# Optimization experiments

Hardware: AMD Instinct MI355X
Metric: run time of the kernel (lower is better)

## Reference

```python
import jax, jax.numpy as jnp
import numpy as np
from jax import lax

B, H, W, CIN = 32, 64, 64, 128
F, KH, KW = 256, 3, 3
NCLS = 10


def setup_inputs() -> dict:
    key = jax.random.key(0)
    k1, k2, k3, k4 = jax.random.split(key, 4)
    x = jax.random.normal(k1, (B, H, W, CIN), dtype=jnp.float32)
    classes = jax.random.randint(k2, (B, 1), 0, NCLS, dtype=jnp.int32)
    kernel = jax.random.normal(k3, (NCLS, KH, KW, CIN, F), dtype=jnp.float32) * 0.05
    bias = jax.random.normal(k4, (NCLS, F), dtype=jnp.float32) * 0.05
    return {"x": x, "classes": classes, "kernel": kernel, "bias": bias}


def reference(x, classes, kernel, bias):
    # classes: [B,1] -> [B]
    cls = jnp.squeeze(classes, axis=1)
    k_per = kernel[cls]   # [B, KH, KW, CIN, F] per-sample gathered expert kernel
    b_per = bias[cls]     # [B, F]

    def conv_one(xi, ki):
        # xi: [H,W,CIN], ki: [KH,KW,CIN,F]
        y = lax.conv_general_dilated(
            xi[None], ki,
            window_strides=(1, 1),
            padding="SAME",
            rhs_dilation=(1, 1),
            dimension_numbers=("NHWC", "HWIO", "NHWC"),
        )
        return y[0]

    out = jax.vmap(conv_one)(x, k_per)          # [B,H,W,F]
    out = out + b_per[:, None, None, :]
    return out
```

## Files before the change

kernel.cpp:

```cpp
#include <hip/hip_runtime.h>
#include <stdint.h>

#define BATCH 32
#define CINX 128
#define FOUT 256
#define NCLS 10

typedef __bf16 bf16x8 __attribute__((ext_vector_type(8)));
typedef float f32x4 __attribute__((ext_vector_type(4)));

#define WT_SLAB 32768
#define WT_BYTES ((size_t)NCLS * 9 * WT_SLAB * 2)
#define Z_BYTES 4096
#define X16_BYTES ((size_t)BATCH * 4096 * CINX * 2)
#define WS_NEED (WT_BYTES + Z_BYTES + X16_BYTES)

#define BAR() __builtin_amdgcn_s_barrier()
#define SCHEDBAR() __builtin_amdgcn_sched_barrier(0)
#define VMW4() asm volatile("s_waitcnt vmcnt(4)" ::: "memory")
#define VMW0() asm volatile("s_waitcnt vmcnt(0)" ::: "memory")

__device__ __forceinline__ void gl16(const void* g, void* l) {
    __builtin_amdgcn_global_load_lds(
        (const __attribute__((address_space(1))) void*)g,
        (__attribute__((address_space(3))) void*)l, 16, 0, 0);
}

__global__ __launch_bounds__(256) void prep_all(const float* __restrict__ kin,
                                                __bf16* __restrict__ wt,
                                                const float* __restrict__ x,
                                                __bf16* __restrict__ x16,
                                                __bf16* __restrict__ zbuf) {
    if (blockIdx.x < NCLS * 9) {
        __shared__ __bf16 tile[128 * 260];
        const int slab = blockIdx.x;
        const float* src = kin + (size_t)slab * (CINX * FOUT);
        __bf16* dst = wt + (size_t)slab * WT_SLAB;
        const int t = threadIdx.x;
#pragma unroll
        for (int i = 0; i < 32; ++i) {
            int e4 = t + i * 256;
            int c = e4 >> 6, f4 = e4 & 63;
            f32x4 v = *(const f32x4*)(src + (size_t)e4 * 4);
            __bf16* p = &tile[c * 260 + f4 * 4];
            p[0] = (__bf16)v[0]; p[1] = (__bf16)v[1];
            p[2] = (__bf16)v[2]; p[3] = (__bf16)v[3];
        }
        __syncthreads();
#pragma unroll
        for (int i = 0; i < 16; ++i) {
            int g = t + i * 256;
            int c32 = g >> 10;
            int u = g & 1023;
            int f = u >> 2, slot = u & 3;
            int cu = slot ^ ((f >> 1) & 3);
            int c0 = c32 * 32 + cu * 8;
            bf16x8 o;
#pragma unroll
            for (int j = 0; j < 8; ++j) o[j] = tile[(c0 + j) * 260 + f];
            *(bf16x8*)(dst + (size_t)g * 8) = o;
        }
    } else {
        const int bx = blockIdx.x - NCLS * 9;
        const size_t u = (size_t)bx * 256 + threadIdx.x;
        f32x4 a = *(const f32x4*)(x + u * 8);
        f32x4 c = *(const f32x4*)(x + u * 8 + 4);
        bf16x8 o;
#pragma unroll
        for (int j = 0; j < 4; ++j) { o[j] = (__bf16)a[j]; o[4 + j] = (__bf16)c[j]; }
        *(bf16x8*)(x16 + u * 8) = o;
        if (bx == 0 && threadIdx.x < 128) {
            bf16x8 z;
#pragma unroll
            for (int j = 0; j < 8; ++j) z[j] = (__bf16)0.f;
            *(bf16x8*)(zbuf + (size_t)threadIdx.x * 8) = z;
        }
    }
}

__global__ __launch_bounds__(512, 2) void conv16u(
    const __bf16* __restrict__ xg16, const int* __restrict__ cls_g,
    const __bf16* __restrict__ wt, const float* __restrict__ bias,
    const __bf16* __restrict__ zbuf, float* __restrict__ out) {
    __shared__ __align__(16) char lds[131072];

    const int bid0 = blockIdx.x;
    const int swz  = (bid0 & 7) * 64 + (bid0 >> 3);
    const int b    = swz >> 4;
    const int pt   = swz & 15;
    const int cls  = cls_g[b];
    const int y0   = pt << 2;

    const int tid  = threadIdx.x;
    const int lane = tid & 63;
    const int wid  = tid >> 6;
    const int wm   = wid >> 2;
    const int wn   = wid & 3;
    const int l15  = lane & 15;
    const int l4   = lane >> 4;

    const __bf16* xb   = xg16 + (size_t)b * 4096 * CINX;
    const __bf16* wcls = wt + (size_t)cls * 9 * WT_SLAB;

    const __bf16* PA[2];
    const __bf16* WB[2];
    const __bf16* ZS[2];
    int vmask[2];
    int dstu[2];
#pragma unroll
    for (int i = 0; i < 2; ++i) {
        const int u = i * 512 + tid;
        const int px = u >> 2, slot = u & 3;
        const int py = px >> 6, gx = px & 63;
        const int cuoff = (slot ^ ((px >> 1) & 3)) * 8;
        const int ay = y0 + py;
        PA[i] = xb + ((size_t)(ay * 64 + gx)) * CINX + cuoff;
        WB[i] = wcls + (size_t)u * 8;
        ZS[i] = zbuf + (size_t)(u & 63) * 8;
        dstu[i] = u * 16;
        int m = 0;
#pragma unroll
        for (int tap = 0; tap < 9; ++tap) {
            const int dy = tap / 3 - 1, dx = tap % 3 - 1;
            const int yy = ay + dy, xx = gx + dx;
            m |= ((((unsigned)yy < 64u) && ((unsigned)xx < 64u)) ? 1 : 0) << tap;
        }
        vmask[i] = m;
    }

    int adA[8], adB[4];
#pragma unroll
    for (int mt = 0; mt < 8; ++mt) {
        const int px = wm * 128 + mt * 16 + l15;
        adA[mt] = (px * 4 + (l4 ^ ((px >> 1) & 3))) * 16;
    }
#pragma unroll
    for (int nt = 0; nt < 4; ++nt) {
        const int f = wn * 64 + nt * 16 + l15;
        adB[nt] = 65536 + (f * 4 + (l4 ^ ((f >> 1) & 3))) * 16;
    }

    f32x4 acc[8][4];
#pragma unroll
    for (int i = 0; i < 8; ++i)
#pragma unroll
        for (int j = 0; j < 4; ++j)
#pragma unroll
            for (int r = 0; r < 4; ++r) acc[i][j][r] = 0.f;

    auto stageA = [&](int s2, int kk) {
        const int pk  = (s2 & 1) * 2 + kk;
        const int tap = s2 >> 1;
        const int dy = tap / 3 - 1, dx = tap % 3 - 1;
        const int cq = (s2 & 1) * 2 + kk;
        const int aoff = (dy * 64 + dx) * CINX + cq * 32;
#pragma unroll
        for (int i = 0; i < 2; ++i) {
            const __bf16* src = ((vmask[i] >> tap) & 1) ? (PA[i] + aoff) : ZS[i];
            gl16(src, lds + pk * 16384 + dstu[i]);
        }
    };
    auto stageB = [&](int s2, int kk) {
        const int pk = (s2 & 1) * 2 + kk;
        const int cq = (s2 & 1) * 2 + kk;
        const size_t woff = (size_t)(s2 >> 1) * WT_SLAB + (size_t)cq * 8192;
#pragma unroll
        for (int i = 0; i < 2; ++i)
            gl16(WB[i] + woff, lds + 65536 + pk * 16384 + dstu[i]);
    };

    bf16x8 AA[2][4], BB[2][4];
    auto rdA = [&](int set, int pk, int mh) {
#pragma unroll
        for (int mt = 0; mt < 4; ++mt)
            AA[set][mt] = *(const bf16x8*)(lds + pk * 16384 + adA[mh * 4 + mt]);
    };
    auto rdB = [&](int set, int pk) {
#pragma unroll
        for (int nt = 0; nt < 4; ++nt)
            BB[set][nt] = *(const bf16x8*)(lds + pk * 16384 + adB[nt]);
    };
    auto mm = [&](int aset, int bset, int mh) {
        __builtin_amdgcn_s_setprio(1);
#pragma unroll
        for (int mt = 0; mt < 4; ++mt)
#pragma unroll
            for (int nt = 0; nt < 4; ++nt)
                acc[mh * 4 + mt][nt] = __builtin_amdgcn_mfma_f32_16x16x32_bf16(
                    AA[aset][mt], BB[bset][nt], acc[mh * 4 + mt][nt], 0, 0, 0);
        __builtin_amdgcn_s_setprio(0);
    };

    stageA(0, 0); stageB(0, 0);
    stageA(0, 1); stageB(0, 1);
    VMW4();
    BAR();
    SCHEDBAR();
    rdB(0, 0);
    rdA(0, 0, 0);

#pragma unroll
    for (int s = 0; s < 17; ++s) {
        const int pk0 = (s & 1) * 2;
        const int pk1 = pk0 + 1;
        const int pkn = ((s + 1) & 1) * 2;
        rdA(1, pk0, 1);
        stageA(s + 1, 0);
        mm(0, 0, 0);
        stageB(s + 1, 0);
        VMW4();
        BAR();
        SCHEDBAR();
        rdB(1, pk1);
        rdA(0, pk1, 0);
        mm(1, 0, 1);
        rdA(1, pk1, 1);
        stageA(s + 1, 1);
        mm(0, 1, 0);
        stageB(s + 1, 1);
        VMW4();
        BAR();
        SCHEDBAR();
        rdB(0, pkn);
        rdA(0, pkn, 0);
        mm(1, 1, 1);
    }
    rdA(1, 2, 1);
    mm(0, 0, 0);
    VMW0();
    BAR();
    SCHEDBAR();
    rdB(1, 3);
    rdA(0, 3, 0);
    mm(1, 0, 1);
    rdA(1, 3, 1);
    mm(0, 1, 0);
    mm(1, 1, 1);

    float bv[4];
#pragma unroll
    for (int nt = 0; nt < 4; ++nt)
        bv[nt] = bias[cls * FOUT + wn * 64 + nt * 16 + l15];

    float* ob = out + ((size_t)b * 4096 + (size_t)pt * 256) * FOUT;
#pragma unroll
    for (int mt = 0; mt < 8; ++mt) {
#pragma unroll
        for (int r = 0; r < 4; ++r) {
            const int row = wm * 128 + mt * 16 + l4 * 4 + r;
            float* orow = ob + (size_t)row * FOUT;
#pragma unroll
            for (int nt = 0; nt < 4; ++nt)
                orow[wn * 64 + nt * 16 + l15] = acc[mt][nt][r] + bv[nt];
        }
    }
}

__global__ __launch_bounds__(256) void prep_w_fb(const float* __restrict__ kin,
                                                 __bf16* __restrict__ wt) {
    __shared__ __bf16 tile[128 * 260];
    const int slab = blockIdx.x;
    const float* src = kin + (size_t)slab * (CINX * FOUT);
    __bf16* dst = wt + (size_t)slab * (16 * 256 * 8);
    const int t = threadIdx.x;
#pragma unroll
    for (int i = 0; i < 32; ++i) {
        int e4 = t + i * 256;
        int c = e4 >> 6, f4 = e4 & 63;
        f32x4 v = *(const f32x4*)(src + (size_t)e4 * 4);
        __bf16* p = &tile[c * 260 + f4 * 4];
        p[0] = (__bf16)v[0]; p[1] = (__bf16)v[1];
        p[2] = (__bf16)v[2]; p[3] = (__bf16)v[3];
    }
    __syncthreads();
#pragma unroll
    for (int i = 0; i < 16; ++i) {
        int g = t + i * 256;
        int cu = g >> 8, f = g & 255;
        bf16x8 o;
#pragma unroll
        for (int j = 0; j < 8; ++j) o[j] = tile[(cu * 8 + j) * 260 + f];
        *(bf16x8*)(dst + (size_t)g * 8) = o;
    }
}

__global__ __launch_bounds__(512, 2) void conv_fb(
    const float* __restrict__ xg, const int* __restrict__ cls_g,
    const __bf16* __restrict__ wt, const float* __restrict__ bias,
    float* __restrict__ out) {
    __shared__ __align__(16) __bf16 ldsA[2][8 * 256 * 8];
    __shared__ __align__(16) __bf16 ldsB[2][8 * 256 * 8];
    const int bid0 = blockIdx.x;
    const int swz = (bid0 & 7) * 64 + (bid0 >> 3);
    const int b = swz >> 4, pt = swz & 15;
    const int cls = cls_g[b];
    const int y0 = pt << 2;
    const int tid = threadIdx.x, lane = tid & 63, wid = tid >> 6;
    const int wm = wid >> 2, wn = wid & 3, l15 = lane & 15, l4 = lane >> 4;
    const float* xb = xg + (size_t)b * 4096 * CINX;
    const __bf16* wcls = wt + (size_t)cls * 9 * (16 * 256 * 8);
    const int tpx = tid >> 1, tch = (tid & 1) * 32;
    const int py = tpx >> 6, px_ = tpx & 63;
    f32x4 acc[8][4];
#pragma unroll
    for (int i = 0; i < 8; ++i)
#pragma unroll
        for (int j = 0; j < 4; ++j)
#pragma unroll
            for (int r = 0; r < 4; ++r) acc[i][j][r] = 0.f;
    f32x4 va[8];
    auto issueB = [&](int s, int buf) {
        const int tap = s >> 1, chalf = (s & 1) << 6;
        const __bf16* wsrc = wcls + (size_t)tap * (16 * 256 * 8) + chalf * 256;
#pragma unroll
        for (int i = 0; i < 4; ++i) {
            const int u = i * 512 + tid;
            gl16(wsrc + (size_t)u * 8, &ldsB[buf][(size_t)u * 8]);
        }
    };
    auto issueA = [&](int s) {
        const int tap = s >> 1, chalf = (s & 1) << 6;
        const int dy = tap / 3 - 1, dx = tap % 3 - 1;
        const int gy = y0 + py + dy, gx = px_ + dx;
        const bool valid = ((unsigned)gy < 64u) && ((unsigned)gx < 64u);
        const float* src = xb + ((size_t)(gy * 64 + gx)) * CINX + chalf + tch;
        if (valid) {
#pragma unroll
            for (int j2 = 0; j2 < 8; ++j2) va[j2] = *(const f32x4*)(src + j2 * 4);
        } else {
#pragma unroll
            for (int j2 = 0; j2 < 8; ++j2)
#pragma unroll
                for (int q = 0; q < 4; ++q) va[j2][q] = 0.f;
        }
    };
    auto writeA = [&](int buf) {
#pragma unroll
        for (int j = 0; j < 4; ++j) {
            bf16x8 pk;
#pragma unroll
            for (int q = 0; q < 4; ++q) {
                pk[q] = (__bf16)va[2 * j][q];
                pk[4 + q] = (__bf16)va[2 * j + 1][q];
            }
            const int u = ((tid & 1) * 4 + j) * 256 + tpx;
            *(bf16x8*)(&ldsA[buf][(size_t)u * 8]) = pk;
        }
    };
    auto compute = [&](int buf) {
#pragma unroll
        for (int kk = 0; kk < 2; ++kk) {
            const int cu = kk * 4 + l4;
            bf16x8 afr[8], bfr[4];
#pragma unroll
            for (int mt = 0; mt < 8; ++mt)
                afr[mt] = *(const bf16x8*)(
                    &ldsA[buf][(size_t)(cu * 256 + wm * 128 + mt * 16 + l15) * 8]);
#pragma unroll
            for (int nt = 0; nt < 4; ++nt)
                bfr[nt] = *(const bf16x8*)(
                    &ldsB[buf][(size_t)(cu * 256 + wn * 64 + nt * 16 + l15) * 8]);
#pragma unroll
            for (int mt = 0; mt < 8; ++mt)
#pragma unroll
                for (int nt = 0; nt < 4; ++nt)
                    acc[mt][nt] = __builtin_amdgcn_mfma_f32_16x16x32_bf16(
                        afr[mt], bfr[nt], acc[mt][nt], 0, 0, 0);
        }
    };
    issueB(0, 0);
    issueA(0);
    writeA(0);
    __syncthreads();
    int cur = 0;
    for (int s = 0; s < 17; ++s) {
        issueB(s + 1, cur ^ 1);
        issueA(s + 1);
        compute(cur);
        writeA(cur ^ 1);
        __syncthreads();
        cur ^= 1;
    }
    compute(cur);
    float bv[4];
#pragma unroll
    for (int nt = 0; nt < 4; ++nt)
        bv[nt] = bias[cls * FOUT + wn * 64 + nt * 16 + l15];
    float* ob = out + ((size_t)b * 4096 + (size_t)pt * 256) * FOUT;
#pragma unroll
    for (int mt = 0; mt < 8; ++mt) {
#pragma unroll
        for (int r = 0; r < 4; ++r) {
            const int row = wm * 128 + mt * 16 + l4 * 4 + r;
            float* orow = ob + (size_t)row * FOUT;
#pragma unroll
            for (int nt = 0; nt < 4; ++nt)
                orow[wn * 64 + nt * 16 + l15] = acc[mt][nt][r] + bv[nt];
        }
    }
}

extern "C" void kernel_launch(void* const* d_in, const int* in_sizes, int n_in,
                              void* d_out, int out_size, void* d_ws, size_t ws_size,
                              hipStream_t stream) {
    const float* x       = (const float*)d_in[0];
    const int*   classes = (const int*)d_in[1];
    const float* kin     = (const float*)d_in[2];
    const float* bias    = (const float*)d_in[3];
    float* out = (float*)d_out;

    char* ws = (char*)d_ws;
    __bf16* wt   = (__bf16*)ws;
    __bf16* zbuf = (__bf16*)(ws + WT_BYTES);
    __bf16* x16  = (__bf16*)(ws + WT_BYTES + Z_BYTES);

    if (ws_size >= WS_NEED) {
        prep_all<<<dim3(NCLS * 9 + 8192), dim3(256), 0, stream>>>(kin, wt, x,
                                                                  x16, zbuf);
        conv16u<<<dim3(512), dim3(512), 0, stream>>>(x16, classes, wt, bias,
                                                     zbuf, out);
    } else {
        prep_w_fb<<<dim3(NCLS * 9), dim3(256), 0, stream>>>(kin, wt);
        conv_fb<<<dim3(512), dim3(512), 0, stream>>>(x, classes, wt, bias, out);
    }
}
```

Measured before the change: 97.76 us.

## Use 4-wave blocks with 128x128 warp tiles in per-class conv GEMM

New measurement: 98.79 us. About the same (+1.0%).

```diff
diff --git a/kernel.cpp b/kernel.cpp
--- a/kernel.cpp
+++ b/kernel.cpp
@@ -17,7 +17,7 @@
 
 #define BAR() __builtin_amdgcn_s_barrier()
 #define SCHEDBAR() __builtin_amdgcn_sched_barrier(0)
-#define VMW4() asm volatile("s_waitcnt vmcnt(4)" ::: "memory")
+#define VMW8() asm volatile("s_waitcnt vmcnt(8)" ::: "memory")
 #define VMW0() asm volatile("s_waitcnt vmcnt(0)" ::: "memory")
 
 __device__ __forceinline__ void gl16(const void* g, void* l) {
@@ -78,7 +78,7 @@
     }
 }
 
-__global__ __launch_bounds__(512, 2) void conv16u(
+__global__ __launch_bounds__(256, 1) void conv4w(
     const __bf16* __restrict__ xg16, const int* __restrict__ cls_g,
     const __bf16* __restrict__ wt, const float* __restrict__ bias,
     const __bf16* __restrict__ zbuf, float* __restrict__ out) {
@@ -94,57 +94,39 @@
     const int tid  = threadIdx.x;
     const int lane = tid & 63;
     const int wid  = tid >> 6;
-    const int wm   = wid >> 2;
-    const int wn   = wid & 3;
+    const int wm   = wid >> 1;
+    const int wn   = wid & 1;
     const int l15  = lane & 15;
     const int l4   = lane >> 4;
 
     const __bf16* xb   = xg16 + (size_t)b * 4096 * CINX;
     const __bf16* wcls = wt + (size_t)cls * 9 * WT_SLAB;
 
-    const __bf16* PA[2];
-    const __bf16* WB[2];
-    const __bf16* ZS[2];
-    int vmask[2];
-    int dstu[2];
-#pragma unroll
-    for (int i = 0; i < 2; ++i) {
-        const int u = i * 512 + tid;
-        const int px = u >> 2, slot = u & 3;
-        const int py = px >> 6, gx = px & 63;
-        const int cuoff = (slot ^ ((px >> 1) & 3)) * 8;
-        const int ay = y0 + py;
-        PA[i] = xb + ((size_t)(ay * 64 + gx)) * CINX + cuoff;
-        WB[i] = wcls + (size_t)u * 8;
-        ZS[i] = zbuf + (size_t)(u & 63) * 8;
-        dstu[i] = u * 16;
-        int m = 0;
-#pragma unroll
-        for (int tap = 0; tap < 9; ++tap) {
-            const int dy = tap / 3 - 1, dx = tap % 3 - 1;
-            const int yy = ay + dy, xx = gx + dx;
-            m |= ((((unsigned)yy < 64u) && ((unsigned)xx < 64u)) ? 1 : 0) << tap;
-        }
-        vmask[i] = m;
-    }
-
-    int adA[8], adB[4];
+    const int gx   = tid >> 2;
+    const int slot = tid & 3;
+    const int cuoff = (slot ^ ((gx >> 1) & 3)) * 8;
+    const __bf16* PA0 = xb + ((size_t)(y0 * 64 + gx)) * CINX + cuoff;
+    const char*   ZS  = (const char*)zbuf + tid * 16;
+    const int vym = ((y0 > 0) ? 1 : 0) | 0x1E | ((y0 < 60 ? 1 : 0) << 5);
+    const int vxm = ((gx >= 1) ? 1 : 0) | 2 | ((gx <= 62 ? 1 : 0) << 2);
+
+    int adA[8], adB[8];
 #pragma unroll
     for (int mt = 0; mt < 8; ++mt) {
         const int px = wm * 128 + mt * 16 + l15;
         adA[mt] = (px * 4 + (l4 ^ ((px >> 1) & 3))) * 16;
     }
 #pragma unroll
-    for (int nt = 0; nt < 4; ++nt) {
-        const int f = wn * 64 + nt * 16 + l15;
+    for (int nt = 0; nt < 8; ++nt) {
+        const int f = wn * 128 + nt * 16 + l15;
         adB[nt] = 65536 + (f * 4 + (l4 ^ ((f >> 1) & 3))) * 16;
     }
 
-    f32x4 acc[8][4];
+    f32x4 acc[8][8];
 #pragma unroll
     for (int i = 0; i < 8; ++i)
 #pragma unroll
-        for (int j = 0; j < 4; ++j)
+        for (int j = 0; j < 8; ++j)
 #pragma unroll
             for (int r = 0; r < 4; ++r) acc[i][j][r] = 0.f;
 
@@ -155,9 +137,11 @@
         const int cq = (s2 & 1) * 2 + kk;
         const int aoff = (dy * 64 + dx) * CINX + cq * 32;
 #pragma unroll
-        for (int i = 0; i < 2; ++i) {
-            const __bf16* src = ((vmask[i] >> tap) & 1) ? (PA[i] + aoff) : ZS[i];
-            gl16(src, lds + pk * 16384 + dstu[i]);
+        for (int i = 0; i < 4; ++i) {
+            const int ok = ((vym >> (i + dy + 1)) & (vxm >> (dx + 1)) & 1);
+            const void* src = ok ? (const void*)(PA0 + i * 8192 + aoff)
+                                 : (const void*)ZS;
+            gl16(src, lds + pk * 16384 + (i * 256 + tid) * 16);
         }
     };
     auto stageB = [&](int s2, int kk) {
@@ -165,82 +149,81 @@
         const int cq = (s2 & 1) * 2 + kk;
         const size_t woff = (size_t)(s2 >> 1) * WT_SLAB + (size_t)cq * 8192;
 #pragma unroll
-        for (int i = 0; i < 2; ++i)
-            gl16(WB[i] + woff, lds + 65536 + pk * 16384 + dstu[i]);
-    };
-
-    bf16x8 AA[2][4], BB[2][4];
-    auto rdA = [&](int set, int pk, int mh) {
-#pragma unroll
-        for (int mt = 0; mt < 4; ++mt)
-            AA[set][mt] = *(const bf16x8*)(lds + pk * 16384 + adA[mh * 4 + mt]);
-    };
-    auto rdB = [&](int set, int pk) {
+        for (int i = 0; i < 4; ++i)
+            gl16(wcls + woff + (size_t)(i * 256 + tid) * 8,
+                 lds + 65536 + pk * 16384 + (i * 256 + tid) * 16);
+    };
+
+    bf16x8 AS[2][8], BS[2][4];
+    auto rdA = [&](int set, int pk) {
+#pragma unroll
+        for (int mt = 0; mt < 8; ++mt)
+            AS[set][mt] = *(const bf16x8*)(lds + pk * 16384 + adA[mt]);
+    };
+    auto rdB = [&](int set, int pk, int nh) {
 #pragma unroll
         for (int nt = 0; nt < 4; ++nt)
-            BB[set][nt] = *(const bf16x8*)(lds + pk * 16384 + adB[nt]);
-    };
-    auto mm = [&](int aset, int bset, int mh) {
-        __builtin_amdgcn_s_setprio(1);
-#pragma unroll
-        for (int mt = 0; mt < 4; ++mt)
+            BS[set][nt] = *(const bf16x8*)(lds + pk * 16384 + adB[nh * 4 + nt]);
+    };
+    auto mm = [&](int aset, int bset, int nh) {
+#pragma unroll
+        for (int mt = 0; mt < 8; ++mt)
 #pragma unroll
             for (int nt = 0; nt < 4; ++nt)
-                acc[mh * 4 + mt][nt] = __builtin_amdgcn_mfma_f32_16x16x32_bf16(
-                    AA[aset][mt], BB[bset][nt], acc[mh * 4 + mt][nt], 0, 0, 0);
-        __builtin_amdgcn_s_setprio(0);
+                acc[mt][nh * 4 + nt] = __builtin_amdgcn_mfma_f32_16x16x32_bf16(
+                    AS[aset][mt], BS[bset][nt], acc[mt][nh * 4 + nt], 0, 0, 0);
     };
 
     stageA(0, 0); stageB(0, 0);
     stageA(0, 1); stageB(0, 1);
-    VMW4();
+    VMW8();
     BAR();
     SCHEDBAR();
-    rdB(0, 0);
-    rdA(0, 0, 0);
+    rdA(0, 0);
+    rdB(0, 0, 0);
 
 #pragma unroll
     for (int s = 0; s < 17; ++s) {
         const int pk0 = (s & 1) * 2;
         const int pk1 = pk0 + 1;
         const int pkn = ((s + 1) & 1) * 2;
-        rdA(1, pk0, 1);
+        rdB(1, pk0, 1);
         stageA(s + 1, 0);
         mm(0, 0, 0);
         stageB(s + 1, 0);
-        VMW4();
+        VMW8();
         BAR();
         SCHEDBAR();
-        rdB(1, pk1);
-        rdA(0, pk1, 0);
-        mm(1, 0, 1);
-        rdA(1, pk1, 1);
+        rdA(1, pk1);
+        rdB(0, pk1, 0);
+        mm(0, 1, 1);
+        rdB(1, pk1, 1);
         stageA(s + 1, 1);
-        mm(0, 1, 0);
+        mm(1, 0, 0);
         stageB(s + 1, 1);
-        VMW4();
+        VMW8();
         BAR();
         SCHEDBAR();
-        rdB(0, pkn);
-        rdA(0, pkn, 0);
+        rdA(0, pkn);
+        rdB(0, pkn, 0);
         mm(1, 1, 1);
     }
-    rdA(1, 2, 1);
+    rdB(1, 2, 1);
     mm(0, 0, 0);
     VMW0();
     BAR();
     SCHEDBAR();
-    rdB(1, 3);
-    rdA(0, 3, 0);
-    mm(1, 0, 1);
-    rdA(1, 3, 1);
-    mm(0, 1, 0);
+    rdA(1, 3);
+    rdB(0, 3, 0);
+    mm(0, 1, 1);
+    rdB(1, 3, 1);
+    mm(1, 0, 0);
     mm(1, 1, 1);
 
-    float bv[4];
-#pragma unroll
-    for (int nt = 0; nt < 4; ++nt)
-        bv[nt] = bias[cls * FOUT + wn * 64 + nt * 16 + l15];
+    float bv[8];
+#pragma unroll
+    for (int nt = 0; nt < 8; ++nt)
+        bv[nt] = bias[cls * FOUT + wn * 128 + nt * 16 + l15];
 
     float* ob = out + ((size_t)b * 4096 + (size_t)pt * 256) * FOUT;
 #pragma unroll
@@ -250,8 +233,8 @@
             const int row = wm * 128 + mt * 16 + l4 * 4 + r;
             float* orow = ob + (size_t)row * FOUT;
 #pragma unroll
-            for (int nt = 0; nt < 4; ++nt)
-                orow[wn * 64 + nt * 16 + l15] = acc[mt][nt][r] + bv[nt];
+            for (int nt = 0; nt < 8; ++nt)
+                orow[wn * 128 + nt * 16 + l15] = acc[mt][nt][r] + bv[nt];
         }
     }
 }
@@ -417,8 +400,8 @@
     if (ws_size >= WS_NEED) {
         prep_all<<<dim3(NCLS * 9 + 8192), dim3(256), 0, stream>>>(kin, wt, x,
                                                                   x16, zbuf);
-        conv16u<<<dim3(512), dim3(512), 0, stream>>>(x16, classes, wt, bias,
-                                                     zbuf, out);
+        conv4w<<<dim3(512), dim3(256), 0, stream>>>(x16, classes, wt, bias,
+                                                    zbuf, out);
     } else {
         prep_w_fb<<<dim3(NCLS * 9), dim3(256), 0, stream>>>(kin, wt);
         conv_fb<<<dim3(512), dim3(512), 0, stream>>>(x, classes, wt, bias, out);
```

## Process two output tiles per block, overlapping second tile prefetch with first epilogue

Applied to the files above, without the earlier changes.

New measurement: 142.0 us. 45.3% more time.

```diff
diff --git a/kernel.cpp b/kernel.cpp
--- a/kernel.cpp
+++ b/kernel.cpp
@@ -18,6 +18,7 @@
 #define BAR() __builtin_amdgcn_s_barrier()
 #define SCHEDBAR() __builtin_amdgcn_sched_barrier(0)
 #define VMW4() asm volatile("s_waitcnt vmcnt(4)" ::: "memory")
+#define VMW8() asm volatile("s_waitcnt vmcnt(8)" ::: "memory")
 #define VMW0() asm volatile("s_waitcnt vmcnt(0)" ::: "memory")
 
 __device__ __forceinline__ void gl16(const void* g, void* l) {
@@ -78,18 +79,16 @@
     }
 }
 
-__global__ __launch_bounds__(512, 2) void conv16u(
+__global__ __launch_bounds__(512, 2) void conv2t(
     const __bf16* __restrict__ xg16, const int* __restrict__ cls_g,
     const __bf16* __restrict__ wt, const float* __restrict__ bias,
     const __bf16* __restrict__ zbuf, float* __restrict__ out) {
     __shared__ __align__(16) char lds[131072];
 
     const int bid0 = blockIdx.x;
-    const int swz  = (bid0 & 7) * 64 + (bid0 >> 3);
-    const int b    = swz >> 4;
-    const int pt   = swz & 15;
-    const int cls  = cls_g[b];
-    const int y0   = pt << 2;
+    const int swz  = (bid0 & 7) * 32 + (bid0 >> 3);
+    const int b    = swz >> 3;
+    const int ptp  = swz & 7;
 
     const int tid  = threadIdx.x;
     const int lane = tid & 63;
@@ -99,34 +98,43 @@
     const int l15  = lane & 15;
     const int l4   = lane >> 4;
 
+    const int cls = cls_g[b];
     const __bf16* xb   = xg16 + (size_t)b * 4096 * CINX;
     const __bf16* wcls = wt + (size_t)cls * 9 * WT_SLAB;
 
-    const __bf16* PA[2];
     const __bf16* WB[2];
     const __bf16* ZS[2];
-    int vmask[2];
-    int dstu[2];
+    int dstu[2], pxA[2];
 #pragma unroll
     for (int i = 0; i < 2; ++i) {
         const int u = i * 512 + tid;
-        const int px = u >> 2, slot = u & 3;
-        const int py = px >> 6, gx = px & 63;
-        const int cuoff = (slot ^ ((px >> 1) & 3)) * 8;
-        const int ay = y0 + py;
-        PA[i] = xb + ((size_t)(ay * 64 + gx)) * CINX + cuoff;
         WB[i] = wcls + (size_t)u * 8;
         ZS[i] = zbuf + (size_t)(u & 63) * 8;
         dstu[i] = u * 16;
-        int m = 0;
-#pragma unroll
-        for (int tap = 0; tap < 9; ++tap) {
-            const int dy = tap / 3 - 1, dx = tap % 3 - 1;
-            const int yy = ay + dy, xx = gx + dx;
-            m |= ((((unsigned)yy < 64u) && ((unsigned)xx < 64u)) ? 1 : 0) << tap;
-        }
-        vmask[i] = m;
-    }
+        pxA[i] = u >> 2;
+    }
+    const __bf16* PA[2];
+    int vmask[2];
+    auto setup_tile = [&](int y0) {
+#pragma unroll
+        for (int i = 0; i < 2; ++i) {
+            const int u = i * 512 + tid;
+            const int px = pxA[i], slot = u & 3;
+            const int py = px >> 6, gx = px & 63;
+            const int cuoff = (slot ^ ((px >> 1) & 3)) * 8;
+            const int ay = y0 + py;
+            PA[i] = xb + ((size_t)(ay * 64 + gx)) * CINX + cuoff;
+            int m = 0;
+#pragma unroll
+            for (int tap = 0; tap < 9; ++tap) {
+                const int dy = tap / 3 - 1, dx = tap % 3 - 1;
+                const int yy = ay + dy, xx = gx + dx;
+                m |= ((((unsigned)yy < 64u) && ((unsigned)xx < 64u)) ? 1 : 0)
+                     << tap;
+            }
+            vmask[i] = m;
+        }
+    };
 
     int adA[8], adB[4];
 #pragma unroll
@@ -191,6 +199,29 @@
         __builtin_amdgcn_s_setprio(0);
     };
 
+    float bv[4];
+#pragma unroll
+    for (int nt = 0; nt < 4; ++nt)
+        bv[nt] = bias[cls * FOUT + wn * 64 + nt * 16 + l15];
+
+    auto store_tile = [&](int pt) {
+        float* ob = out + ((size_t)b * 4096 + (size_t)pt * 256) * FOUT;
+#pragma unroll
+        for (int mt = 0; mt < 8; ++mt) {
+#pragma unroll
+            for (int r = 0; r < 4; ++r) {
+                const int row = wm * 128 + mt * 16 + l4 * 4 + r;
+                float* orow = ob + (size_t)row * FOUT;
+#pragma unroll
+                for (int nt = 0; nt < 4; ++nt)
+                    orow[wn * 64 + nt * 16 + l15] = acc[mt][nt][r] + bv[nt];
+            }
+        }
+    };
+
+    const int pt_a = ptp * 2, pt_b = ptp * 2 + 1;
+
+    setup_tile(pt_a << 2);
     stageA(0, 0); stageB(0, 0);
     stageA(0, 1); stageB(0, 1);
     VMW4();
@@ -227,6 +258,61 @@
     }
     rdA(1, 2, 1);
     mm(0, 0, 0);
+    setup_tile(pt_b << 2);
+    stageA(0, 0); stageB(0, 0);
+    stageA(0, 1); stageB(0, 1);
+    VMW8();
+    BAR();
+    SCHEDBAR();
+    rdB(1, 3);
+    rdA(0, 3, 0);
+    mm(1, 0, 1);
+    rdA(1, 3, 1);
+    mm(0, 1, 0);
+    mm(1, 1, 1);
+
+    VMW4();
+    BAR();
+    SCHEDBAR();
+    rdB(0, 0);
+    rdA(0, 0, 0);
+
+    store_tile(pt_a);
+#pragma unroll
+    for (int i = 0; i < 8; ++i)
+#pragma unroll
+        for (int j = 0; j < 4; ++j)
+#pragma unroll
+            for (int r = 0; r < 4; ++r) acc[i][j][r] = 0.f;
+
+#pragma unroll
+    for (int s = 0; s < 17; ++s) {
+        const int pk0 = (s & 1) * 2;
+        const int pk1 = pk0 + 1;
+        const int pkn = ((s + 1) & 1) * 2;
+        rdA(1, pk0, 1);
+        stageA(s + 1, 0);
+        mm(0, 0, 0);
+        stageB(s + 1, 0);
+        VMW4();
+        BAR();
+        SCHEDBAR();
+        rdB(1, pk1);
+        rdA(0, pk1, 0);
+        mm(1, 0, 1);
+        rdA(1, pk1, 1);
+        stageA(s + 1, 1);
+        mm(0, 1, 0);
+        stageB(s + 1, 1);
+        VMW4();
+        BAR();
+        SCHEDBAR();
+        rdB(0, pkn);
+        rdA(0, pkn, 0);
+        mm(1, 1, 1);
+    }
+    rdA(1, 2, 1);
+    mm(0, 0, 0);
     VMW0();
     BAR();
     SCHEDBAR();
@@ -237,23 +323,7 @@
     mm(0, 1, 0);
     mm(1, 1, 1);
 
-    float bv[4];
-#pragma unroll
-    for (int nt = 0; nt < 4; ++nt)
-        bv[nt] = bias[cls * FOUT + wn * 64 + nt * 16 + l15];
-
-    float* ob = out + ((size_t)b * 4096 + (size_t)pt * 256) * FOUT;
-#pragma unroll
-    for (int mt = 0; mt < 8; ++mt) {
-#pragma unroll
-        for (int r = 0; r < 4; ++r) {
-            const int row = wm * 128 + mt * 16 + l4 * 4 + r;
-            float* orow = ob + (size_t)row * FOUT;
-#pragma unroll
-            for (int nt = 0; nt < 4; ++nt)
-                orow[wn * 64 + nt * 16 + l15] = acc[mt][nt][r] + bv[nt];
-        }
-    }
+    store_tile(pt_b);
 }
 
 __global__ __launch_bounds__(256) void prep_w_fb(const float* __restrict__ kin,
@@ -417,8 +487,8 @@
     if (ws_size >= WS_NEED) {
         prep_all<<<dim3(NCLS * 9 + 8192), dim3(256), 0, stream>>>(kin, wt, x,
                                                                   x16, zbuf);
-        conv16u<<<dim3(512), dim3(512), 0, stream>>>(x16, classes, wt, bias,
-                                                     zbuf, out);
+        conv2t<<<dim3(256), dim3(512), 0, stream>>>(x16, classes, wt, bias,
+                                                    zbuf, out);
     } else {
         prep_w_fb<<<dim3(NCLS * 9), dim3(256), 0, stream>>>(kin, wt);
         conv_fb<<<dim3(512), dim3(512), 0, stream>>>(x, classes, wt, bias, out);
```
